# Kernel tuning notes

Measured on AMD Instinct MI355X. Metric: run time of the kernel, lower is better.

## Reference

```python
import jax, jax.numpy as jnp
import numpy as np

N_PTS = 2000   # n: number of Z1 samples (rows of K_Z1Z1)
Z_PTS = 2000   # z: number of Z2 samples (cols of K_Z1Z2 / gammas)
A_SAMP = 1000  # a: number of alpha samples
D = 8          # d: treatment dimension


def setup_inputs() -> dict:
    key = jax.random.key(0)
    ks = jax.random.split(key, 8)
    M = jax.random.normal(ks[0], (N_PTS, D), jnp.float32)
    N = jax.random.normal(ks[1], (N_PTS, D), jnp.float32)
    X = (M + N) / 2  # initial_X in the torch module (the nn.Parameter)
    # PSD kernel matrix so the ridge solve is well conditioned
    A = jax.random.normal(ks[2], (N_PTS, N_PTS), jnp.float32)
    K_Z1Z1 = (A @ A.T) / N_PTS
    K_Z1Z2 = jax.random.normal(ks[3], (N_PTS, Z_PTS), jnp.float32) * 0.1
    gamma_MN = jax.random.normal(ks[4], (N_PTS, Z_PTS), jnp.float32) * 0.01
    # offset keeps the complex denominator exps @ gamma_N away from zero
    gamma_N = jax.random.normal(ks[5], (N_PTS, Z_PTS), jnp.float32) * 0.01 + 1.0 / N_PTS
    alpha_samples = jax.random.normal(ks[6], (A_SAMP, D), jnp.float32)
    log_lambda_X = jnp.zeros((1,), jnp.float32)  # log(lambda_N) with lambda_N = 1.0
    return {
        "M": M, "N": N, "X": X, "log_lambda_X": log_lambda_X,
        "K_Z1Z1": K_Z1Z1, "K_Z1Z2": K_Z1Z2,
        "gamma_MN": gamma_MN, "gamma_N": gamma_N,
        "alpha_samples": alpha_samples,
    }


def _compute_labels(alpha, exponent, gamma_num, gamma_den, mult_num):
    # exps: [a, n] complex64 phase features exp(i * <alpha, exponent_j>)
    exps = jnp.exp(1j * (alpha @ exponent.T))
    # denominator: [a, z]
    denom = exps @ gamma_den.astype(jnp.complex64)
    # numerator: [a, z, d]
    num = jnp.einsum('jd,jz,aj->azd',
                     mult_num.astype(jnp.complex64),
                     gamma_num.astype(jnp.complex64),
                     exps)
    return num / denom[:, :, None]


def reference(M, N, X, log_lambda_X, K_Z1Z1, K_Z1Z2, gamma_MN, gamma_N, alpha_samples):
    n = K_Z1Z1.shape[0]
    # kernel ridge solve: gamma_X = (K + n*exp(log_lambda)*I)^{-1} K_Z1Z2  -> [n, z]
    reg = n * jnp.exp(log_lambda_X[0])
    gamma_X = jnp.linalg.solve(K_Z1Z1 + reg * jnp.eye(n, dtype=K_Z1Z1.dtype), K_Z1Z2)
    MN_labels = _compute_labels(alpha_samples, N, gamma_MN, gamma_N, M)   # [a, z, d]
    X_labels = _compute_labels(alpha_samples, X, gamma_X, gamma_X, X)     # [a, z, d]
    diff = MN_labels - X_labels
    # torch.linalg.norm(., dim=-1)**2 on complex == sum |.|^2 over d
    loss = jnp.mean(jnp.sum(jnp.abs(diff) ** 2, axis=-1))
    return loss
```

## Files before the change

kernel.cpp:

```cpp
#include <hip/hip_runtime.h>


typedef __bf16 bf16;
typedef __bf16 bf16x8 __attribute__((ext_vector_type(8)));
typedef float f32x4 __attribute__((ext_vector_type(4)));
typedef int i32x8 __attribute__((ext_vector_type(8)));
typedef int i32x4 __attribute__((ext_vector_type(4)));

#define AS1 __attribute__((address_space(1)))
#define AS3 __attribute__((address_space(3)))

__device__ __forceinline__ void async16(const void* g, void* l) {
  __builtin_amdgcn_global_load_lds((AS1 const unsigned int*)g,
                                   (AS3 unsigned int*)l, 16, 0, 0);
}

__device__ __forceinline__ unsigned int pk4f8(float a, float b, float c,
                                              float d) {
  int w = __builtin_amdgcn_cvt_pk_fp8_f32(a, b, 0, false);
  w = __builtin_amdgcn_cvt_pk_fp8_f32(c, d, w, true);
  return (unsigned int)w;
}

__device__ __forceinline__ i32x8 ld_swz32(const unsigned char* rowp, int kg,
                                          int fsw) {
  i32x4 lo = *(const i32x4*)(rowp + (kg ^ fsw));
  i32x4 hi = *(const i32x4*)(rowp + ((kg + 16) ^ fsw));
  i32x8 v;
  v[0] = lo[0]; v[1] = lo[1]; v[2] = lo[2]; v[3] = lo[3];
  v[4] = hi[0]; v[5] = hi[1]; v[6] = hi[2]; v[7] = hi[3];
  return v;
}

__device__ __forceinline__ void stage64x64(const float* __restrict__ src,
                                           int row0, int col0,
                                           float (*t)[65], int tid) {
#pragma unroll
  for (int it = 0; it < 4; ++it) {
    int e = it * 256 + tid;
    int r = e >> 4, c4 = (e & 15) * 4;
    float4 v = {0.f, 0.f, 0.f, 0.f};
    if (row0 + r < 2000 && col0 + c4 < 2000)
      v = *(const float4*)(src + (size_t)(row0 + r) * 2000 + col0 + c4);
    t[r][c4] = v.x; t[r][c4 + 1] = v.y; t[r][c4 + 2] = v.z; t[r][c4 + 3] = v.w;
  }
}

__device__ __forceinline__ void build_mn(const float* __restrict__ gMN,
                                         const float* __restrict__ Mm,
                                         unsigned char* __restrict__ B8,
                                         int j0, int zl0, int zg0, int ZC,
                                         int tid, float (*t)[65]) {
  const size_t PL = (size_t)ZC * 2048;
  int zg = zg0 + zl0;
  stage64x64(gMN, j0, zg, t, tid);
  __syncthreads();
  const float4* M4 = (const float4*)Mm;
#pragma unroll
  for (int it = 0; it < 2; ++it) {
    int idx = it * 256 + tid;
    int zr = idx >> 3, c8 = (idx & 7) * 8;
    float g[8], mrow[8][8];
#pragma unroll
    for (int e = 0; e < 8; ++e) {
      g[e] = 64.f * t[c8 + e][zr];
      int jj = j0 + c8 + e;
      if (jj < 2000) {
        float4 ma = M4[jj * 2], mb = M4[jj * 2 + 1];
        mrow[e][0] = ma.x; mrow[e][1] = ma.y; mrow[e][2] = ma.z;
        mrow[e][3] = ma.w; mrow[e][4] = mb.x; mrow[e][5] = mb.y;
        mrow[e][6] = mb.z; mrow[e][7] = mb.w;
      } else {
#pragma unroll
        for (int d = 0; d < 8; ++d) mrow[e][d] = 0.f;
      }
    }
    size_t ob = (size_t)(zl0 + zr) * 2048 + j0 + c8;
#pragma unroll
    for (int d = 0; d < 8; ++d) {
      uint2 u;
      u.x = pk4f8(g[0] * mrow[0][d], g[1] * mrow[1][d], g[2] * mrow[2][d],
                  g[3] * mrow[3][d]);
      u.y = pk4f8(g[4] * mrow[4][d], g[5] * mrow[5][d], g[6] * mrow[6][d],
                  g[7] * mrow[7][d]);
      *(uint2*)(B8 + (size_t)d * PL + ob) = u;
    }
  }
}

__device__ __forceinline__ void build_x(const bf16* __restrict__ gxHi,
                                        const bf16* __restrict__ gxLo,
                                        const float* __restrict__ Xm,
                                        unsigned char* __restrict__ B8,
                                        int j0, int zl0, int zg0, int ZC,
                                        int tid) {
  const size_t PL = (size_t)ZC * 2048;
  const float4* X4 = (const float4*)Xm;
#pragma unroll
  for (int it = 0; it < 2; ++it) {
    int idx = it * 256 + tid;
    int zr = idx >> 3, c8 = (idx & 7) * 8;
    size_t gb = (size_t)(zg0 + zl0 + zr) * 2048 + j0 + c8;
    bf16x8 vh = *(const bf16x8*)(gxHi + gb);
    bf16x8 vl = *(const bf16x8*)(gxLo + gb);
    float gx[8], xr[8][8];
#pragma unroll
    for (int e = 0; e < 8; ++e) {
      gx[e] = 8192.f * ((float)vh[e] + (float)vl[e]);
      int jj = j0 + c8 + e;
      if (jj < 2000) {
        float4 xa = X4[jj * 2], xb = X4[jj * 2 + 1];
        xr[e][0] = xa.x; xr[e][1] = xa.y; xr[e][2] = xa.z; xr[e][3] = xa.w;
        xr[e][4] = xb.x; xr[e][5] = xb.y; xr[e][6] = xb.z; xr[e][7] = xb.w;
      } else {
#pragma unroll
        for (int d = 0; d < 8; ++d) xr[e][d] = 0.f;
      }
    }
    size_t ob = (size_t)(zl0 + zr) * 2048 + j0 + c8;
#pragma unroll
    for (int d = 0; d < 8; ++d) {
      uint2 u;
      u.x = pk4f8(gx[0] * xr[0][d], gx[1] * xr[1][d], gx[2] * xr[2][d],
                  gx[3] * xr[3][d]);
      u.y = pk4f8(gx[4] * xr[4][d], gx[5] * xr[5][d], gx[6] * xr[6][d],
                  gx[7] * xr[7][d]);
      *(uint2*)(B8 + (size_t)(8 + d) * PL + ob) = u;
    }
  }
}

__global__ __launch_bounds__(256) void k_cvt(
    const float* __restrict__ K11, const float* __restrict__ K12,
    const float* __restrict__ gN, bf16* __restrict__ Kbf,
    bf16* __restrict__ K12T, bf16* __restrict__ K12TL,
    bf16* __restrict__ BtNh, bf16* __restrict__ BtNl,
    float* __restrict__ out) {
  __shared__ float t[64][65];
  const int bid = blockIdx.x, tid = threadIdx.x;
  if (bid < 2048) {
    if (bid == 0 && tid == 0) out[0] = 0.f;
    int e = (bid * 256 + tid) * 8;
    int j = e >> 11, k = e & 2047;
    bf16x8 v;
    if (j < 2000 && k < 2000) {
      const float4* s = (const float4*)(K11 + (size_t)j * 2000 + k);
      float4 f0 = s[0], f1 = s[1];
      v[0] = (bf16)f0.x; v[1] = (bf16)f0.y; v[2] = (bf16)f0.z; v[3] = (bf16)f0.w;
      v[4] = (bf16)f1.x; v[5] = (bf16)f1.y; v[6] = (bf16)f1.z; v[7] = (bf16)f1.w;
    } else {
      for (int i = 0; i < 8; ++i) v[i] = (bf16)0.f;
    }
    *(bf16x8*)(Kbf + e) = v;
  } else {
    bool isK12 = bid < 3072;
    const float* src = isK12 ? K12 : gN;
    bf16* dh = isK12 ? K12T : BtNh;
    bf16* dl = isK12 ? K12TL : BtNl;
    int b2 = bid - (isK12 ? 2048 : 3072);
    int j0 = (b2 & 31) * 64, z0 = (b2 >> 5) * 64;
    stage64x64(src, j0, z0, t, tid);
    __syncthreads();
#pragma unroll
    for (int it = 0; it < 2; ++it) {
      int idx = it * 256 + tid;
      int zr = idx >> 3, c8 = (idx & 7) * 8;
      bf16x8 vh, vl;
#pragma unroll
      for (int e = 0; e < 8; ++e) {
        float g = t[c8 + e][zr];
        bf16 h = (bf16)g;
        vh[e] = h;
        vl[e] = (bf16)(g - (float)h);
      }
      size_t ob = (size_t)(z0 + zr) * 2048 + j0 + c8;
      *(bf16x8*)(dh + ob) = vh;
      *(bf16x8*)(dl + ob) = vl;
    }
  }
}

__global__ __launch_bounds__(256, 2) void k_big(
    const bf16* __restrict__ K12T, const bf16* __restrict__ K12TL,
    const bf16* __restrict__ Kbf, const float* __restrict__ ll,
    const float* __restrict__ al, const float* __restrict__ Nm,
    const float* __restrict__ Xm, const float* __restrict__ gMN,
    const float* __restrict__ Mm, bf16* __restrict__ gxHi,
    bf16* __restrict__ gxLo, bf16* __restrict__ AphH,
    bf16* __restrict__ AphL, unsigned char* __restrict__ Aph8,
    unsigned char* __restrict__ B8, int ZC) {
  __shared__ __align__(16) char smem[34816];
  const int tid = threadIdx.x;
  const int bid = blockIdx.x;
  if (bid >= 1536) {
    int pid = bid - 1536;
    build_mn(gMN, Mm, B8, (pid & 31) * 64, (pid >> 5) * 64, 0, ZC, tid,
             (float(*)[65])smem);
    return;
  }
  if (bid >= 512) {
    const size_t PA = (size_t)1024 * 2048;
    int a = bid - 512;
    int j0 = tid * 8;
    float vc[4][8];
    if (a < 1000) {
      const float4* A4 = (const float4*)al;
      const float4* N4 = (const float4*)Nm;
      const float4* X4 = (const float4*)Xm;
      float4 a0 = A4[a * 2], a1 = A4[a * 2 + 1];
#pragma unroll
      for (int e = 0; e < 8; ++e) {
        int j = j0 + e;
        if (j < 2000) {
          float4 n0 = N4[j * 2], n1 = N4[j * 2 + 1];
          float4 x0 = X4[j * 2], x1 = X4[j * 2 + 1];
          float pn = a0.x * n0.x + a0.y * n0.y + a0.z * n0.z + a0.w * n0.w +
                     a1.x * n1.x + a1.y * n1.y + a1.z * n1.z + a1.w * n1.w;
          float px = a0.x * x0.x + a0.y * x0.y + a0.z * x0.z + a0.w * x0.w +
                     a1.x * x1.x + a1.y * x1.y + a1.z * x1.z + a1.w * x1.w;
          __sincosf(pn, &vc[1][e], &vc[0][e]);
          __sincosf(px, &vc[3][e], &vc[2][e]);
        } else {
          vc[0][e] = vc[1][e] = vc[2][e] = vc[3][e] = 0.f;
        }
      }
    } else {
#pragma unroll
      for (int p = 0; p < 4; ++p)
#pragma unroll
        for (int e = 0; e < 8; ++e) vc[p][e] = 0.f;
    }
    size_t o = (size_t)a * 2048 + j0;
#pragma unroll
    for (int p = 0; p < 4; ++p) {
      bf16x8 vh, vl;
#pragma unroll
      for (int e = 0; e < 8; ++e) {
        bf16 h = (bf16)vc[p][e];
        vh[e] = h;
        vl[e] = (bf16)(vc[p][e] - (float)h);
      }
      *(bf16x8*)(AphH + p * PA + o) = vh;
      *(bf16x8*)(AphL + p * PA + o) = vl;
      uint2 u8;
      u8.x = pk4f8(vc[p][0], vc[p][1], vc[p][2], vc[p][3]);
      u8.y = pk4f8(vc[p][4], vc[p][5], vc[p][6], vc[p][7]);
      *(uint2*)(Aph8 + p * PA + o) = u8;
    }
    return;
  }
  bf16(*lds)[64] = (bf16(*)[64])smem;
  int wrk = (bid & 7) * 64 + (bid >> 3);
  int bm = (wrk >> 5) * 128;
  int bn = (wrk & 31) * 64;
  const int w = tid >> 6, ln = tid & 63;
  const int fr = ln & 15, kq = (ln >> 4) * 8;
  const int esw = (fr & 7) << 3;
  const int r32 = tid >> 3, c8 = (tid & 7) * 8;
  f32x4 acc[4][2];
#pragma unroll
  for (int i = 0; i < 4; i++)
#pragma unroll
    for (int jj = 0; jj < 2; jj++) acc[i][jj] = {0.f, 0.f, 0.f, 0.f};
  const int m0 = (w & 1) * 64, n0 = (w >> 1) * 32;
  for (int kt = 0; kt < 2048; kt += 64) {
#pragma unroll
    for (int q = 0; q < 4; ++q) {
      int row = q * 32 + r32;
      int sc = c8 ^ ((row & 7) << 3);
      async16(K12T + (size_t)(bm + row) * 2048 + (kt + sc), &lds[row][c8]);
    }
#pragma unroll
    for (int q = 0; q < 2; ++q) {
      int row = q * 32 + r32;
      int sc = c8 ^ ((row & 7) << 3);
      async16(Kbf + (size_t)(bn + row) * 2048 + (kt + sc),
              &lds[128 + row][c8]);
    }
    __syncthreads();
#pragma unroll
    for (int ks = 0; ks < 64; ks += 32) {
      bf16x8 a[4], b[2];
#pragma unroll
      for (int i = 0; i < 4; i++)
        a[i] = *(const bf16x8*)&lds[m0 + i * 16 + fr][(ks + kq) ^ esw];
#pragma unroll
      for (int jj = 0; jj < 2; jj++)
        b[jj] = *(const bf16x8*)&lds[128 + n0 + jj * 16 + fr][(ks + kq) ^ esw];
      __builtin_amdgcn_s_setprio(1);
#pragma unroll
      for (int i = 0; i < 4; i++)
#pragma unroll
        for (int jj = 0; jj < 2; jj++)
          acc[i][jj] = __builtin_amdgcn_mfma_f32_16x16x32_bf16(
              a[i], b[jj], acc[i][jj], 0, 0, 0);
      __builtin_amdgcn_s_setprio(0);
    }
    __syncthreads();
  }
  float inv = 1.f / (2000.f * __expf(ll[0]));
  float* ft = (float*)smem;
  const int cr = (ln >> 4) * 4, cc = ln & 15;
#pragma unroll
  for (int i = 0; i < 4; i++)
#pragma unroll
    for (int jj = 0; jj < 2; jj++)
#pragma unroll
      for (int r = 0; r < 4; r++)
        ft[(m0 + i * 16 + cr + r) * 66 + n0 + jj * 16 + cc] = acc[i][jj][r];
  __syncthreads();
  const size_t PL = (size_t)ZC * 2048;
  const float4* X4 = (const float4*)Xm;
#pragma unroll
  for (int it = 0; it < 4; ++it) {
    int idx = it * 256 + tid;
    int m = idx >> 3, cg = (idx & 7) * 8;
    size_t gb = (size_t)(bm + m) * 2048 + bn + cg;
    bf16x8 kh = *(const bf16x8*)(K12T + gb);
    bf16x8 klo = *(const bf16x8*)(K12TL + gb);
    bf16x8 vh, vl;
#pragma unroll
    for (int e = 0; e < 8; ++e) {
      float t1 = ft[m * 66 + cg + e];
      float gx = ((float)kh[e] + (float)klo[e] - t1 * inv) * inv;
      bf16 hh = (bf16)gx;
      vh[e] = hh;
      vl[e] = (bf16)(gx - (float)hh);
    }
    *(bf16x8*)(gxHi + gb) = vh;
    *(bf16x8*)(gxLo + gb) = vl;
    int zg = bm + m;
    if (zg < ZC) {
      float gxq[8], xr[8][8];
#pragma unroll
      for (int e = 0; e < 8; ++e) {
        gxq[e] = 8192.f * ((float)vh[e] + (float)vl[e]);
        int jj = bn + cg + e;
        if (jj < 2000) {
          float4 xa = X4[jj * 2], xb = X4[jj * 2 + 1];
          xr[e][0] = xa.x; xr[e][1] = xa.y; xr[e][2] = xa.z; xr[e][3] = xa.w;
          xr[e][4] = xb.x; xr[e][5] = xb.y; xr[e][6] = xb.z; xr[e][7] = xb.w;
        } else {
#pragma unroll
          for (int d = 0; d < 8; ++d) xr[e][d] = 0.f;
        }
      }
      size_t ob = (size_t)zg * 2048 + bn + cg;
#pragma unroll
      for (int d = 0; d < 8; ++d) {
        uint2 u;
        u.x = pk4f8(gxq[0] * xr[0][d], gxq[1] * xr[1][d], gxq[2] * xr[2][d],
                    gxq[3] * xr[3][d]);
        u.y = pk4f8(gxq[4] * xr[4][d], gxq[5] * xr[5][d], gxq[6] * xr[6][d],
                    gxq[7] * xr[7][d]);
        *(uint2*)(B8 + (size_t)(8 + d) * PL + ob) = u;
      }
    }
  }
}

__global__ __launch_bounds__(256, 2) void k_mm(
    const bf16* __restrict__ AphH, const bf16* __restrict__ AphL,
    const unsigned char* __restrict__ Aph8,
    const unsigned char* __restrict__ B8, const bf16* __restrict__ BtNh,
    const bf16* __restrict__ BtNl, const bf16* __restrict__ gxHi,
    const bf16* __restrict__ gxLo, unsigned int* __restrict__ Cpk,
    float* __restrict__ den, int ZC, int zg0) {
  const size_t PA = (size_t)1024 * 2048;
  const size_t PL8 = (size_t)ZC * 2048;
  const size_t PC = (size_t)1024 * ZC;
  __shared__ __align__(16) bf16 smem[3 * 128 * 64];
  const int tid = threadIdx.x;
  const int w = tid >> 6, ln = tid & 63;
  const int fr = ln & 15;
  const int cr = (ln >> 4) * 4, cc = ln & 15;

  const int BYT = ZC >> 7;
  const int nyT = ZC >> 6;
  const int xcd = blockIdx.x & 7;
  const int slot = blockIdx.x >> 3;
  const int numSlots = 16 * BYT;

  if (slot < numSlots) {
    const int half = numSlots >> 1;
    int zb = xcd * 2 + (slot >= half ? 1 : 0);
    int rem = slot & (half - 1);
    int bn = (rem >> 3) * 128;
    int bm = (rem & 7) * 128;

    unsigned char* l8 = (unsigned char*)smem;
    const unsigned char* A0 = Aph8 + (size_t)(zb < 8 ? 0 : 2) * PA;
    const unsigned char* A1 = A0 + PA;
    const unsigned char* B = B8 + (size_t)zb * PL8;
    const int sb = (zb < 8) ? 0x79797979 : 0x72727272;
    unsigned int* P = Cpk + (size_t)zb * PC;
    const int colb = (ln & 7) * 16;
    const int kg = (ln >> 4) * 32;
    const int fsw = (fr & 7) << 4;

    f32x4 acc0[4][4], acc1[4][4];
#pragma unroll
    for (int i = 0; i < 4; i++)
#pragma unroll
      for (int j = 0; j < 4; j++) {
        acc0[i][j] = {0.f, 0.f, 0.f, 0.f};
        acc1[i][j] = {0.f, 0.f, 0.f, 0.f};
      }
    const int m0 = (w & 1) * 64, n0 = (w >> 1) * 64;

    for (int kt = 0; kt < 2048; kt += 128) {
#pragma unroll
      for (int q = 0; q < 4; ++q) {
        int row = w * 32 + q * 8 + (ln >> 3);
        int sc = colb ^ ((row & 7) << 4);
        async16(A0 + (size_t)(bm + row) * 2048 + kt + sc,
                l8 + row * 128 + colb);
        async16(A1 + (size_t)(bm + row) * 2048 + kt + sc,
                l8 + 16384 + row * 128 + colb);
        async16(B + (size_t)(bn + row) * 2048 + kt + sc,
                l8 + 32768 + row * 128 + colb);
      }
      __syncthreads();
      i32x8 a0[4], a1[4];
#pragma unroll
      for (int i = 0; i < 4; i++) {
        const unsigned char* pr = l8 + (m0 + i * 16 + fr) * 128;
        a0[i] = ld_swz32(pr, kg, fsw);
        a1[i] = ld_swz32(pr + 16384, kg, fsw);
      }
      __builtin_amdgcn_s_setprio(1);
#pragma unroll
      for (int j = 0; j < 4; ++j) {
        i32x8 bfv =
            ld_swz32(l8 + 32768 + (n0 + j * 16 + fr) * 128, kg, fsw);
#pragma unroll
        for (int i = 0; i < 4; ++i) {
          acc0[i][j] = __builtin_amdgcn_mfma_scale_f32_16x16x128_f8f6f4(
              a0[i], bfv, acc0[i][j], 0, 0, 0, 0x7F7F7F7F, 0, sb);
          acc1[i][j] = __builtin_amdgcn_mfma_scale_f32_16x16x128_f8f6f4(
              a1[i], bfv, acc1[i][j], 0, 0, 0, 0x7F7F7F7F, 0, sb);
        }
      }
      __builtin_amdgcn_s_setprio(0);
      __syncthreads();
    }
#pragma unroll
    for (int i = 0; i < 4; i++)
#pragma unroll
      for (int j = 0; j < 4; j++)
#pragma unroll
        for (int r = 0; r < 4; r++) {
          union { bf16 h[2]; unsigned int u; } pk;
          pk.h[0] = (bf16)acc0[i][j][r];
          pk.h[1] = (bf16)acc1[i][j][r];
          P[(size_t)(bm + m0 + i * 16 + cr + r) * ZC +
            (bn + n0 + j * 16 + cc)] = pk.u;
        }
  } else {
    bf16(*lds)[64] = (bf16(*)[64])smem;
    const int kq = (ln >> 4) * 8;
    const int esw = (fr & 7) << 3;
    int j = slot - numSlots;
    int p = xcd >> 1;
    int ny = (xcd & 1) * (nyT >> 1) + (j >> 3);
    int side = p >> 1, trig = p & 1;
    const bf16* Ah = AphH + (size_t)(side * 2 + trig) * PA;
    const bf16* Al = AphL + (size_t)(side * 2 + trig) * PA;
    const bf16* Bh = (side ? gxHi : BtNh) + (size_t)zg0 * 2048;
    const bf16* Bl = (side ? gxLo : BtNl) + (size_t)zg0 * 2048;
    float* C = den + (size_t)p * PC;
    int bm = (j & 7) * 128, bn = ny * 64;
    const int r32 = tid >> 3, c8 = (tid & 7) * 8;

    f32x4 acc[4][2];
#pragma unroll
    for (int i = 0; i < 4; i++)
#pragma unroll
      for (int jj = 0; jj < 2; jj++) acc[i][jj] = {0.f, 0.f, 0.f, 0.f};
    const int m0 = (w & 1) * 64, n0 = (w >> 1) * 32;

    for (int kt = 0; kt < 2048; kt += 64) {
#pragma unroll
      for (int q = 0; q < 4; ++q) {
        int row = q * 32 + r32;
        int sc = c8 ^ ((row & 7) << 3);
        async16(Ah + (size_t)(bm + row) * 2048 + (kt + sc), &lds[row][c8]);
        async16(Al + (size_t)(bm + row) * 2048 + (kt + sc),
                &lds[128 + row][c8]);
      }
#pragma unroll
      for (int q = 0; q < 2; ++q) {
        int row = q * 32 + r32;
        int sc = c8 ^ ((row & 7) << 3);
        async16(Bh + (size_t)(bn + row) * 2048 + (kt + sc),
                &lds[256 + row][c8]);
        async16(Bl + (size_t)(bn + row) * 2048 + (kt + sc),
                &lds[320 + row][c8]);
      }
      __syncthreads();
#pragma unroll
      for (int ks = 0; ks < 64; ks += 32) {
        bf16x8 ah[4], alo[4], bh[2], blo[2];
#pragma unroll
        for (int i = 0; i < 4; i++) {
          ah[i]  = *(const bf16x8*)&lds[m0 + i * 16 + fr][(ks + kq) ^ esw];
          alo[i] =
              *(const bf16x8*)&lds[128 + m0 + i * 16 + fr][(ks + kq) ^ esw];
        }
#pragma unroll
        for (int jj = 0; jj < 2; jj++) {
          bh[jj] =
              *(const bf16x8*)&lds[256 + n0 + jj * 16 + fr][(ks + kq) ^ esw];
          blo[jj] =
              *(const bf16x8*)&lds[320 + n0 + jj * 16 + fr][(ks + kq) ^ esw];
        }
        __builtin_amdgcn_s_setprio(1);
#pragma unroll
        for (int i = 0; i < 4; i++)
#pragma unroll
          for (int jj = 0; jj < 2; jj++) {
            acc[i][jj] = __builtin_amdgcn_mfma_f32_16x16x32_bf16(
                alo[i], bh[jj], acc[i][jj], 0, 0, 0);
            acc[i][jj] = __builtin_amdgcn_mfma_f32_16x16x32_bf16(
                ah[i], blo[jj], acc[i][jj], 0, 0, 0);
            acc[i][jj] = __builtin_amdgcn_mfma_f32_16x16x32_bf16(
                ah[i], bh[jj], acc[i][jj], 0, 0, 0);
          }
        __builtin_amdgcn_s_setprio(0);
      }
      __syncthreads();
    }
#pragma unroll
    for (int i = 0; i < 4; i++)
#pragma unroll
      for (int jj = 0; jj < 2; jj++)
#pragma unroll
        for (int r = 0; r < 4; r++) {
          size_t idx = (size_t)(bm + m0 + i * 16 + cr + r) * ZC +
                       (bn + n0 + jj * 16 + cc);
          C[idx] = acc[i][jj][r];
        }
  }
}

__device__ __forceinline__ void load8p(const unsigned int* p, float* re,
                                       float* im) {
  uint4 u0 = ((const uint4*)p)[0], u1 = ((const uint4*)p)[1];
  re[0] = __uint_as_float(u0.x << 16); im[0] = __uint_as_float(u0.x & 0xffff0000u);
  re[1] = __uint_as_float(u0.y << 16); im[1] = __uint_as_float(u0.y & 0xffff0000u);
  re[2] = __uint_as_float(u0.z << 16); im[2] = __uint_as_float(u0.z & 0xffff0000u);
  re[3] = __uint_as_float(u0.w << 16); im[3] = __uint_as_float(u0.w & 0xffff0000u);
  re[4] = __uint_as_float(u1.x << 16); im[4] = __uint_as_float(u1.x & 0xffff0000u);
  re[5] = __uint_as_float(u1.y << 16); im[5] = __uint_as_float(u1.y & 0xffff0000u);
  re[6] = __uint_as_float(u1.z << 16); im[6] = __uint_as_float(u1.z & 0xffff0000u);
  re[7] = __uint_as_float(u1.w << 16); im[7] = __uint_as_float(u1.w & 0xffff0000u);
}
__device__ __forceinline__ void load8d(const float* p, float* o) {
  float4 f0 = ((const float4*)p)[0], f1 = ((const float4*)p)[1];
  o[0] = f0.x; o[1] = f0.y; o[2] = f0.z; o[3] = f0.w;
  o[4] = f1.x; o[5] = f1.y; o[6] = f1.z; o[7] = f1.w;
}

__global__ __launch_bounds__(256) void k_redprep(
    const unsigned int* __restrict__ Cpk, const float* __restrict__ den,
    float* __restrict__ out, const float* __restrict__ gMN,
    const float* __restrict__ Mm, const bf16* __restrict__ gxHi,
    const bf16* __restrict__ gxLo, const float* __restrict__ Xm,
    unsigned char* __restrict__ B8Next, int ZC, int zg0) {
  __shared__ float sm[64][65];
  const int bid = blockIdx.x, tid = threadIdx.x;
  if (bid >= 500) {
    int pid = bid - 500;
    int j0 = (pid & 31) * 64, zl0 = (pid >> 5) * 64;
    int zg0n = zg0 + ZC;
    build_mn(gMN, Mm, B8Next, j0, zl0, zg0n, ZC, tid, sm);
    build_x(gxHi, gxLo, Xm, B8Next, j0, zl0, zg0n, ZC, tid);
    return;
  }
  const size_t PS = (size_t)1024 * ZC;
  int a = bid * 2 + (tid >> 7);
  int zt = tid & 127;
  float acc = 0.f;
  for (int z = zt * 8; z < ZC; z += 1024) {
    if (zg0 + z >= 2000) break;
    size_t base = (size_t)a * ZC + z;
    float mdr[8], mdi[8], xdr[8], xdi[8], im[8], ix[8];
    load8d(den + 0 * PS + base, mdr);
    load8d(den + 1 * PS + base, mdi);
    load8d(den + 2 * PS + base, xdr);
    load8d(den + 3 * PS + base, xdi);
#pragma unroll
    for (int e = 0; e < 8; ++e) {
      im[e] = 1.f / (mdr[e] * mdr[e] + mdi[e] * mdi[e]);
      ix[e] = 1.f / (xdr[e] * xdr[e] + xdi[e] * xdi[e]);
    }
#pragma unroll
    for (int d = 0; d < 8; ++d) {
      float ar[8], ai[8], br[8], bi[8];
      load8p(Cpk + (size_t)d * PS + base, ar, ai);
      load8p(Cpk + (size_t)(8 + d) * PS + base, br, bi);
#pragma unroll
      for (int e = 0; e < 8; ++e) {
        float r1 = (ar[e] * mdr[e] + ai[e] * mdi[e]) * im[e];
        float i1 = (ai[e] * mdr[e] - ar[e] * mdi[e]) * im[e];
        float r2 = (br[e] * xdr[e] + bi[e] * xdi[e]) * ix[e];
        float i2 = (bi[e] * xdr[e] - br[e] * xdi[e]) * ix[e];
        float dr = r1 - r2, di = i1 - i2;
        acc += dr * dr + di * di;
      }
    }
  }
  for (int off = 32; off; off >>= 1) acc += __shfl_down(acc, off, 64);
  __shared__ float red[4];
  if (!(tid & 63)) red[tid >> 6] = acc;
  __syncthreads();
  if (!tid)
    atomicAdd(out, (red[0] + red[1] + red[2] + red[3]) * (1.f / 2000000.f));
}

extern "C" void kernel_launch(void* const* d_in, const int* in_sizes, int n_in,
                              void* d_out, int out_size, void* d_ws,
                              size_t ws_size, hipStream_t stream) {
  const float* Mm  = (const float*)d_in[0];
  const float* Nm  = (const float*)d_in[1];
  const float* Xm  = (const float*)d_in[2];
  const float* ll  = (const float*)d_in[3];
  const float* K11 = (const float*)d_in[4];
  const float* K12 = (const float*)d_in[5];
  const float* gMN = (const float*)d_in[6];
  const float* gN  = (const float*)d_in[7];
  const float* al  = (const float*)d_in[8];

  char* ws = (char*)d_ws;
  const size_t MB = 1024 * 1024;
  bf16* AphH = (bf16*)(ws);
  bf16* AphL = (bf16*)(ws + 16 * MB);
  unsigned char* Aph8 = (unsigned char*)(ws + 32 * MB);
  bf16* gxHi = (bf16*)(ws + 40 * MB);
  bf16* gxLo = (bf16*)(ws + 48 * MB);
  bf16* BtNh = (bf16*)(ws + 56 * MB);
  bf16* BtNl = (bf16*)(ws + 64 * MB);
  char* chunkRgn = ws + 72 * MB;

  size_t fixedNeed = 96 * MB;
  size_t avail = (ws_size > fixedNeed) ? ws_size - fixedNeed : 0;
  int ZC = 2048;
  while (ZC > 128 && (size_t)114688 * ZC > avail) ZC >>= 1;
  int NC = 2048 / ZC;
  unsigned char* B8c = (unsigned char*)(chunkRgn);
  float* denc = (float*)(chunkRgn + (size_t)32768 * ZC);
  unsigned int* Cpkc = (unsigned int*)(chunkRgn + (size_t)49152 * ZC);
  char* trans = chunkRgn + (size_t)114688 * ZC;
  bf16* Kbf   = (bf16*)(trans);
  bf16* K12T  = (bf16*)(trans + 8 * MB);
  bf16* K12TL = (bf16*)(trans + 16 * MB);

  int NBP = 32 * (ZC / 64);
  int GMM = 192 * (ZC >> 7);

  k_cvt<<<dim3(4096), dim3(256), 0, stream>>>(K11, K12, gN, Kbf, K12T, K12TL,
                                              BtNh, BtNl, (float*)d_out);
  k_big<<<dim3(1536 + NBP), dim3(256), 0, stream>>>(
      K12T, K12TL, Kbf, ll, al, Nm, Xm, gMN, Mm, gxHi, gxLo, AphH, AphL, Aph8,
      B8c, ZC);
  for (int c = 0; c < NC; ++c) {
    int zg0 = c * ZC;
    k_mm<<<dim3(GMM), dim3(256), 0, stream>>>(
        AphH, AphL, Aph8, B8c, BtNh, BtNl, gxHi, gxLo, Cpkc, denc, ZC, zg0);
    int nblk = (c + 1 < NC) ? 500 + NBP : 500;
    k_redprep<<<dim3(nblk), dim3(256), 0, stream>>>(
        Cpkc, denc, (float*)d_out, gMN, Mm, gxHi, gxLo, Xm, B8c, ZC, zg0);
  }
  (void)in_sizes; (void)n_in; (void)out_size;
}
```

Before: 451.8 us.

## Move phase-feature and MN-B build from k_big into interleaved k_cvt roles

The independent work (alpha phase features sin/cos, and the MN B-operand build) moves out of the GEMM kernel k_big into the conversion kernel k_cvt. Blocks there are interleaved by role (bid%6) so memory-bound conversion and compute-bound trig work share the GPU at the same time. k_big now launches only its 512 GEMM blocks, which removes tail imbalance between heterogeneous block types. The risk is that k_cvt grows to 6144 blocks with its build_mn role limited by ZC, and the LDS buffer is reused with a different type.

```diff
diff --git a/kernel.cpp b/kernel.cpp
--- a/kernel.cpp
+++ b/kernel.cpp
@@ -135,12 +135,18 @@
     const float* __restrict__ gN, bf16* __restrict__ Kbf,
     bf16* __restrict__ K12T, bf16* __restrict__ K12TL,
     bf16* __restrict__ BtNh, bf16* __restrict__ BtNl,
-    float* __restrict__ out) {
+    const float* __restrict__ al, const float* __restrict__ Nm,
+    const float* __restrict__ Xm, bf16* __restrict__ AphH,
+    bf16* __restrict__ AphL, unsigned char* __restrict__ Aph8,
+    const float* __restrict__ gMN, const float* __restrict__ Mm,
+    unsigned char* __restrict__ B8, int ZC, float* __restrict__ out) {
   __shared__ float t[64][65];
   const int bid = blockIdx.x, tid = threadIdx.x;
-  if (bid < 2048) {
-    if (bid == 0 && tid == 0) out[0] = 0.f;
-    int e = (bid * 256 + tid) * 8;
+  const int role = bid % 6, rid = bid / 6;
+  if (role < 2) {
+    int kid = rid * 2 + role;
+    if (kid == 0 && tid == 0) out[0] = 0.f;
+    int e = (kid * 256 + tid) * 8;
     int j = e >> 11, k = e & 2047;
     bf16x8 v;
     if (j < 2000 && k < 2000) {
@@ -152,12 +158,12 @@
       for (int i = 0; i < 8; ++i) v[i] = (bf16)0.f;
     }
     *(bf16x8*)(Kbf + e) = v;
-  } else {
-    bool isK12 = bid < 3072;
+  } else if (role < 4) {
+    bool isK12 = (role == 2);
     const float* src = isK12 ? K12 : gN;
     bf16* dh = isK12 ? K12T : BtNh;
     bf16* dl = isK12 ? K12TL : BtNl;
-    int b2 = bid - (isK12 ? 2048 : 3072);
+    int b2 = rid;
     int j0 = (b2 & 31) * 64, z0 = (b2 >> 5) * 64;
     stage64x64(src, j0, z0, t, tid);
     __syncthreads();
@@ -177,30 +183,9 @@
       *(bf16x8*)(dh + ob) = vh;
       *(bf16x8*)(dl + ob) = vl;
     }
-  }
-}
-
-__global__ __launch_bounds__(256, 2) void k_big(
-    const bf16* __restrict__ K12T, const bf16* __restrict__ K12TL,
-    const bf16* __restrict__ Kbf, const float* __restrict__ ll,
-    const float* __restrict__ al, const float* __restrict__ Nm,
-    const float* __restrict__ Xm, const float* __restrict__ gMN,
-    const float* __restrict__ Mm, bf16* __restrict__ gxHi,
-    bf16* __restrict__ gxLo, bf16* __restrict__ AphH,
-    bf16* __restrict__ AphL, unsigned char* __restrict__ Aph8,
-    unsigned char* __restrict__ B8, int ZC) {
-  __shared__ __align__(16) char smem[34816];
-  const int tid = threadIdx.x;
-  const int bid = blockIdx.x;
-  if (bid >= 1536) {
-    int pid = bid - 1536;
-    build_mn(gMN, Mm, B8, (pid & 31) * 64, (pid >> 5) * 64, 0, ZC, tid,
-             (float(*)[65])smem);
-    return;
-  }
-  if (bid >= 512) {
+  } else if (role == 4) {
     const size_t PA = (size_t)1024 * 2048;
-    int a = bid - 512;
+    int a = rid;
     int j0 = tid * 8;
     float vc[4][8];
     if (a < 1000) {
@@ -247,8 +232,21 @@
       u8.y = pk4f8(vc[p][4], vc[p][5], vc[p][6], vc[p][7]);
       *(uint2*)(Aph8 + p * PA + o) = u8;
     }
-    return;
-  }
+  } else {
+    int pid = rid;
+    if (pid >= 32 * (ZC >> 6)) return;
+    build_mn(gMN, Mm, B8, (pid & 31) * 64, (pid >> 5) * 64, 0, ZC, tid, t);
+  }
+}
+
+__global__ __launch_bounds__(256, 2) void k_big(
+    const bf16* __restrict__ K12T, const bf16* __restrict__ K12TL,
+    const bf16* __restrict__ Kbf, const float* __restrict__ ll,
+    const float* __restrict__ Xm, bf16* __restrict__ gxHi,
+    bf16* __restrict__ gxLo, unsigned char* __restrict__ B8, int ZC) {
+  __shared__ __align__(16) char smem[34816];
+  const int tid = threadIdx.x;
+  const int bid = blockIdx.x;
   bf16(*lds)[64] = (bf16(*)[64])smem;
   int wrk = (bid & 7) * 64 + (bid >> 3);
   int bm = (wrk >> 5) * 128;
@@ -658,11 +656,11 @@
   int NBP = 32 * (ZC / 64);
   int GMM = 192 * (ZC >> 7);
 
-  k_cvt<<<dim3(4096), dim3(256), 0, stream>>>(K11, K12, gN, Kbf, K12T, K12TL,
-                                              BtNh, BtNl, (float*)d_out);
-  k_big<<<dim3(1536 + NBP), dim3(256), 0, stream>>>(
-      K12T, K12TL, Kbf, ll, al, Nm, Xm, gMN, Mm, gxHi, gxLo, AphH, AphL, Aph8,
-      B8c, ZC);
+  k_cvt<<<dim3(6144), dim3(256), 0, stream>>>(
+      K11, K12, gN, Kbf, K12T, K12TL, BtNh, BtNl, al, Nm, Xm, AphH, AphL,
+      Aph8, gMN, Mm, B8c, ZC, (float*)d_out);
+  k_big<<<dim3(512), dim3(256), 0, stream>>>(K12T, K12TL, Kbf, ll, Xm, gxHi,
+                                             gxLo, B8c, ZC);
   for (int c = 0; c < NC; ++c) {
     int zg0 = c * ZC;
     k_mm<<<dim3(GMM), dim3(256), 0, stream>>>(
```

After: 476.0 us. 1.05x slower.
